# Performance work log

Hardware: AMD Instinct MI355X
Metric: run time of the kernel (lower is better)

Reference implementation:

```python
import jax, jax.numpy as jnp
import numpy as np
from jax import lax

D_MODEL = 768
D_STATE = 64
D_CONV = 4
EXPAND = 2
HEADDIM = 64
D_INNER = EXPAND * D_MODEL          # 1536
NHEADS = D_INNER // HEADDIM          # 24
NGROUPS = 1
CONV_DIM = D_INNER + 2 * NGROUPS * D_STATE      # 1664
D_IN_PROJ = 2 * D_INNER + 2 * NGROUPS * D_STATE + NHEADS  # 3224
EPS = 1e-5


def setup_inputs() -> dict:
    key = jax.random.key(0)
    ks = jax.random.split(key, 8)
    B, L = 2, 4096
    x = jax.random.normal(ks[0], (B, L, D_MODEL), jnp.float32)
    W_in = jax.random.normal(ks[1], (D_MODEL, D_IN_PROJ), jnp.float32) * (D_MODEL ** -0.5)
    conv_w = jax.random.normal(ks[2], (CONV_DIM, D_CONV), jnp.float32) * 0.2
    conv_b = jnp.zeros((CONV_DIM,), jnp.float32)
    # dt_bias so that softplus(dt_bias) ~ [1e-3, 1e-1], like mamba init
    dt = jax.random.uniform(ks[3], (NHEADS,), jnp.float32, 1e-3, 1e-1)
    dt_bias = dt + jnp.log(-jnp.expm1(-dt))
    A_log = jnp.log(jax.random.uniform(ks[4], (NHEADS,), jnp.float32, 1.0, 16.0))
    D = jnp.ones((NHEADS,), jnp.float32)
    norm_w = jnp.ones((D_INNER,), jnp.float32)
    W_out = jax.random.normal(ks[5], (D_INNER, D_MODEL), jnp.float32) * (D_INNER ** -0.5)
    return {"x": x, "W_in": W_in, "conv_w": conv_w, "conv_b": conv_b,
            "dt_bias": dt_bias, "A_log": A_log, "D": D,
            "norm_w": norm_w, "W_out": W_out}


def _mamba2(x, W_in, conv_w, conv_b, dt_bias, A_log, D, norm_w, W_out):
    B, L, _ = x.shape
    zxbcdt = x @ W_in                                  # (B,L,3224)
    z = zxbcdt[..., :D_INNER]                          # gate
    xBC = zxbcdt[..., D_INNER:D_INNER + CONV_DIM]
    dt = zxbcdt[..., D_INNER + CONV_DIM:]              # (B,L,H)
    dt = jax.nn.softplus(dt + dt_bias)

    # causal depthwise conv1d, kernel D_CONV, then SiLU
    xp = jnp.pad(xBC, ((0, 0), (D_CONV - 1, 0), (0, 0)))
    conv = sum(xp[:, k:k + L, :] * conv_w[:, k] for k in range(D_CONV))
    xBC = jax.nn.silu(conv + conv_b)

    xs = xBC[..., :D_INNER].reshape(B, L, NHEADS, HEADDIM)
    Bm = xBC[..., D_INNER:D_INNER + D_STATE]           # (B,L,N)
    Cm = xBC[..., D_INNER + D_STATE:]                  # (B,L,N)

    A = -jnp.exp(A_log)                                # (H,)
    dA = jnp.exp(dt * A)                               # (B,L,H)

    def step(h, inp):
        dA_t, dt_t, x_t, B_t, C_t = inp
        # h: (B,H,P,N)
        h = h * dA_t[:, :, None, None] \
            + (dt_t[:, :, None] * x_t)[..., None] * B_t[:, None, None, :]
        y = jnp.einsum('bhpn,bn->bhp', h, C_t)
        return h, y

    inps = (jnp.moveaxis(dA, 1, 0), jnp.moveaxis(dt, 1, 0),
            jnp.moveaxis(xs, 1, 0), jnp.moveaxis(Bm, 1, 0),
            jnp.moveaxis(Cm, 1, 0))
    h0 = jnp.zeros((B, NHEADS, HEADDIM, D_STATE), x.dtype)
    _, ys = lax.scan(step, h0, inps)                   # (L,B,H,P)
    y = jnp.moveaxis(ys, 0, 1) + D[None, None, :, None] * xs
    y = y.reshape(B, L, D_INNER)

    # gated RMSNorm: norm(y * silu(z)) * norm_w
    y = y * jax.nn.silu(z)
    y = y * lax.rsqrt(jnp.mean(y * y, axis=-1, keepdims=True) + EPS) * norm_w
    return y @ W_out


def reference(x, W_in, conv_w, conv_b, dt_bias, A_log, D, norm_w, W_out):
    return _mamba2(x, W_in, conv_w, conv_b, dt_bias, A_log, D, norm_w, W_out)
```

## Files before the change

kernel.cpp:

```cpp
#include <hip/hip_runtime.h>

#define B_   2
#define L_   4096
#define DM   768
#define DI   1536
#define DS   64
#define H_   24
#define P_   64
#define CD   1664
#define NPJ  3224
#define N1   3200
#define Q_   64
#define NC   64
#define SP   76
#define HS   72
#define WDS  772
#define CROWS 16

typedef short          bf16x8 __attribute__((ext_vector_type(8)));
typedef _Float16       f16x8  __attribute__((ext_vector_type(8)));
typedef _Float16       f16x4  __attribute__((ext_vector_type(4)));
typedef unsigned short us8    __attribute__((ext_vector_type(8)));
typedef unsigned short us4    __attribute__((ext_vector_type(4)));
typedef float          f32x4  __attribute__((ext_vector_type(4)));

__device__ __forceinline__ unsigned short f2bf(float f) {
  unsigned u = __float_as_uint(f);
  u += 0x7fffu + ((u >> 16) & 1u);
  return (unsigned short)(u >> 16);
}
__device__ __forceinline__ float bf2f(unsigned short u) {
  return __uint_as_float(((unsigned)u) << 16);
}
__device__ __forceinline__ float siluf(float x) { return x / (1.f + expf(-x)); }
__device__ __forceinline__ float softplusf(float x) { return (x > 20.f) ? x : log1pf(expf(x)); }

__device__ __forceinline__ void gload16(const unsigned short* g, unsigned short* l) {
  __builtin_amdgcn_global_load_lds(
      (const __attribute__((address_space(1))) void*)g,
      (__attribute__((address_space(3))) void*)l, 16, 0, 0);
}

__global__ __launch_bounds__(256)
void k_transpose_cast(const float* __restrict__ src, unsigned short* __restrict__ dst,
                      int R, int C)
{
  __shared__ float tile[32][33];
  const int tx = threadIdx.x & 31, ty = threadIdx.x >> 5;
  const int r0 = blockIdx.x * 32, c0 = blockIdx.y * 32;
#pragma unroll
  for (int r = 0; r < 4; ++r) {
    int rr = r0 + ty + r * 8, cc = c0 + tx;
    if (rr < R && cc < C) tile[ty + r * 8][tx] = src[(size_t)rr * C + cc];
  }
  __syncthreads();
#pragma unroll
  for (int r = 0; r < 4; ++r) {
    int orow = c0 + ty + r * 8, ocol = r0 + tx;
    if (orow < C && ocol < R) dst[(size_t)orow * R + ocol] = f2bf(tile[tx][ty + r * 8]);
  }
}

__global__ void k_wdtT(const float* __restrict__ W_in, float* __restrict__ WdtT)
{
  const int idx = blockIdx.x * 256 + threadIdx.x;
  if (idx >= H_ * DM) return;
  const int k = idx / H_, h = idx % H_;
  WdtT[(size_t)h * DM + k] = W_in[(size_t)k * NPJ + N1 + h];
}

template<int BM, int BN, int WM, int WN, bool OUT_BF16>
__global__ __launch_bounds__((BM / WM) * (BN / WN) * 64)
void k_gemm_t(const unsigned short* __restrict__ A, const unsigned short* __restrict__ Bt,
              void* __restrict__ C0v, int ld0, int ncol0,
              void* __restrict__ C1v, int ld1, int K)
{
  constexpr int MI = WM / 16, NI = WN / 16;
  constexpr int WAVES_N = BN / WN;
  constexpr int T  = (BM / WM) * (BN / WN) * 64;
  constexpr int RG = T / 8;
  constexpr int RA = BM / RG, RB = BN / RG;
  const int m0 = blockIdx.x * BM, n0 = blockIdx.y * BN;
  __shared__ unsigned short As[BM][64];
  __shared__ unsigned short Bs[BN][64];
  const int tid  = threadIdx.x;
  const int wave = tid >> 6, lane = tid & 63;
  const int quad = lane >> 4, r16 = lane & 15;
  const int wm = (wave / WAVES_N) * WM, wn = (wave % WAVES_N) * WN;

  const int lr8 = lane >> 3;
  const int csw = ((lane & 7) ^ lr8) * 8;
  const unsigned short* gA = A  + (size_t)(m0 + wave * 8 + lr8) * K + csw;
  const unsigned short* gB = Bt + (size_t)(n0 + wave * 8 + lr8) * K + csw;
  unsigned short* lA = &As[wave * 8][0] + (size_t)lane * 8;
  unsigned short* lB = &Bs[wave * 8][0] + (size_t)lane * 8;

  f32x4 acc[MI][NI];
#pragma unroll
  for (int mi = 0; mi < MI; ++mi)
#pragma unroll
    for (int ni = 0; ni < NI; ++ni) acc[mi][ni] = (f32x4){0.f, 0.f, 0.f, 0.f};

  for (int k0 = 0; k0 < K; k0 += 64) {
#pragma unroll
    for (int r = 0; r < RA; ++r)
      gload16(gA + (size_t)(r * RG) * K + k0, lA + (size_t)r * RG * 64);
#pragma unroll
    for (int r = 0; r < RB; ++r)
      gload16(gB + (size_t)(r * RG) * K + k0, lB + (size_t)r * RG * 64);
    __syncthreads();
    bf16x8 af[MI][2], bfr[NI][2];
#pragma unroll
    for (int mi = 0; mi < MI; ++mi)
#pragma unroll
      for (int ks = 0; ks < 2; ++ks)
        af[mi][ks] = *(const bf16x8*)&As[wm + mi * 16 + r16][((quad + ks * 4) ^ (r16 & 7)) * 8];
#pragma unroll
    for (int ni = 0; ni < NI; ++ni)
#pragma unroll
      for (int ks = 0; ks < 2; ++ks)
        bfr[ni][ks] = *(const bf16x8*)&Bs[wn + ni * 16 + r16][((quad + ks * 4) ^ (r16 & 7)) * 8];
#pragma unroll
    for (int mi = 0; mi < MI; ++mi)
#pragma unroll
      for (int ni = 0; ni < NI; ++ni)
#pragma unroll
        for (int ks = 0; ks < 2; ++ks)
          acc[mi][ni] = __builtin_amdgcn_mfma_f32_16x16x32_bf16(
              af[mi][ks], bfr[ni][ks], acc[mi][ni], 0, 0, 0);
    __syncthreads();
  }
#pragma unroll
  for (int mi = 0; mi < MI; ++mi)
#pragma unroll
    for (int ni = 0; ni < NI; ++ni) {
      int col = n0 + wn + ni * 16 + r16;
      void* dst; int ld, c;
      if (col < ncol0) { dst = C0v; ld = ld0; c = col; }
      else             { dst = C1v; ld = ld1; c = col - ncol0; }
#pragma unroll
      for (int r = 0; r < 4; ++r) {
        int row = m0 + wm + mi * 16 + quad * 4 + r;
        if (OUT_BF16) ((unsigned short*)dst)[(size_t)row * ld + c] = f2bf(acc[mi][ni][r]);
        else          ((float*)dst)[(size_t)row * ld + c] = acc[mi][ni][r];
      }
    }
}

__global__ __launch_bounds__(256)
void k_conv2(const unsigned short* __restrict__ xbc, const float* __restrict__ cw,
             const float* __restrict__ cb, _Float16* __restrict__ xs,
             float* __restrict__ Bm, float* __restrict__ Cm)
{
  const int ch = blockIdx.x * 256 + threadIdx.x;
  if (ch >= CD) return;
  const int r0 = blockIdx.y * CROWS;
  const float w0 = cw[ch * 4], w1 = cw[ch * 4 + 1], w2 = cw[ch * 4 + 2], w3 = cw[ch * 4 + 3];
  const float bias = cb[ch];
  float a, b, c;
  if ((r0 & (L_ - 1)) == 0) {
    a = 0.f; b = 0.f; c = 0.f;
  } else {
    a = bf2f(xbc[(size_t)(r0 - 3) * CD + ch]);
    b = bf2f(xbc[(size_t)(r0 - 2) * CD + ch]);
    c = bf2f(xbc[(size_t)(r0 - 1) * CD + ch]);
  }
#pragma unroll
  for (int i = 0; i < CROWS; ++i) {
    const int lr = r0 + i;
    float d = bf2f(xbc[(size_t)lr * CD + ch]);
    float v = siluf(bias + a * w0 + b * w1 + c * w2 + d * w3);
    a = b; b = c; c = d;
    if (ch < DI)           xs[(size_t)lr * DI + ch] = (_Float16)v;
    else if (ch < DI + DS) Bm[(size_t)lr * DS + (ch - DI)] = v;
    else                   Cm[(size_t)lr * DS + (ch - DI - DS)] = v;
  }
}

__global__ __launch_bounds__(384)
void k_dt2(const float* __restrict__ x, const float* __restrict__ WdtT,
           const float* __restrict__ dt_bias, float* __restrict__ dtv,
           unsigned short* __restrict__ xb)
{
  __shared__ float sW[H_][WDS];
  for (int i = threadIdx.x; i < H_ * DM; i += 384)
    sW[i / DM][i % DM] = WdtT[i];
  const int h = threadIdx.x % H_, rloc = threadIdx.x / H_;
  const int lrow = blockIdx.x * 16 + rloc;
  const float* xr = x + (size_t)lrow * DM;
  __syncthreads();
  float acc = 0.f;
#pragma unroll 8
  for (int k = 0; k < DM; k += 4) {
    f32x4 xv = *(const f32x4*)(xr + k);
    f32x4 wv = *(const f32x4*)&sW[h][k];
    acc += xv[0] * wv[0] + xv[1] * wv[1] + xv[2] * wv[2] + xv[3] * wv[3];
  }
  dtv[(size_t)lrow * H_ + h] = softplusf(acc + dt_bias[h]);
  const float* xi = xr + h * 32;
  unsigned short* xo = xb + (size_t)lrow * DM + h * 32;
#pragma unroll
  for (int j = 0; j < 32; j += 8) {
    f32x4 a = *(const f32x4*)(xi + j);
    f32x4 b = *(const f32x4*)(xi + j + 4);
    us8 o;
#pragma unroll
    for (int e = 0; e < 4; ++e) { o[e] = f2bf(a[e]); o[e + 4] = f2bf(b[e]); }
    *(us8*)(xo + j) = o;
  }
}

__global__ __launch_bounds__(256)
void k_intra(const _Float16* __restrict__ xs, const float* __restrict__ Bm,
             const float* __restrict__ Cm, const float* __restrict__ dtv,
             const float* __restrict__ A_log, const float* __restrict__ Dp,
             float* __restrict__ cumA, _Float16* __restrict__ ytot,
             _Float16* __restrict__ Sbuf)
{
  const int c = blockIdx.x, h = blockIdx.y, bz = blockIdx.z;
  const int gidx = (bz * H_ + h) * NC + c;
  __shared__ _Float16 sCW[Q_][HS];
  __shared__ _Float16 sB [Q_][HS];
  __shared__ _Float16 sBT[Q_][HS];
  __shared__ _Float16 sXT[Q_][HS];
  __shared__ float scum[Q_], sdt[Q_];
  const int tid = threadIdx.x;
  const int rowbase = bz * L_ + c * Q_;

  {
    const int j = tid >> 2, s16 = (tid & 3) * 16;
    if (tid < Q_) {
      const float dtval = dtv[(size_t)(rowbase + tid) * H_ + h];
      sdt[tid] = dtval;
      const float A = -expf(A_log[h]);
      float v = dtval;
#pragma unroll
      for (int off = 1; off < 64; off <<= 1) {
        float o = __shfl_up(v, off, 64);
        if (tid >= off) v += o;
      }
      v *= A;
      scum[tid] = v;
      cumA[(size_t)gidx * Q_ + tid] = v;
    }
    const _Float16* xsrc = xs + (size_t)(rowbase + j) * DI + h * P_ + s16;
    f16x8 xv0 = *(const f16x8*)xsrc;
    f16x8 xv1 = *(const f16x8*)(xsrc + 8);
    f32x4 bv[4], cv[4];
    const float* bsrc = Bm + (size_t)(rowbase + j) * DS + s16;
    const float* csrc = Cm + (size_t)(rowbase + j) * DS + s16;
#pragma unroll
    for (int q = 0; q < 4; ++q) {
      bv[q] = *(const f32x4*)(bsrc + q * 4);
      cv[q] = *(const f32x4*)(csrc + q * 4);
    }
    __syncthreads();
    const float coef = expf(scum[Q_ - 1] - scum[j]) * sdt[j];
    union { f16x8 v; _Float16 e[8]; } pc[2], pb[2];
#pragma unroll
    for (int q = 0; q < 4; ++q)
#pragma unroll
      for (int e = 0; e < 4; ++e) {
        int o = q * 4 + e;
        pc[o >> 3].e[o & 7] = (_Float16)cv[q][e];
        pb[o >> 3].e[o & 7] = (_Float16)bv[q][e];
        sBT[s16 + o][j] = (_Float16)(bv[q][e] * coef);
        sXT[s16 + o][j] = (o < 8) ? xv0[o] : xv1[o - 8];
      }
    *(f16x8*)&sCW[j][s16]     = pc[0].v;
    *(f16x8*)&sCW[j][s16 + 8] = pc[1].v;
    *(f16x8*)&sB [j][s16]     = pb[0].v;
    *(f16x8*)&sB [j][s16 + 8] = pb[1].v;
  }
  __syncthreads();

  const int wave = tid >> 6, lane = tid & 63;
  const int quad = lane >> 4, r16 = lane & 15;
  const int i0 = wave * 16;
  const int irow = i0 + quad * 4;

  f32x4 g[4];
#pragma unroll
  for (int q = 0; q < 4; ++q) g[q] = (f32x4){0.f, 0.f, 0.f, 0.f};
#pragma unroll
  for (int ni = 0; ni < 4; ++ni) {
    if (ni <= wave) {
#pragma unroll
      for (int ks = 0; ks < 2; ++ks)
        g[ni] = __builtin_amdgcn_mfma_f32_16x16x32_f16(
            *(const f16x8*)&sCW[i0 + r16][ks * 32 + quad * 8],
            *(const f16x8*)&sB [ni * 16 + r16][ks * 32 + quad * 8], g[ni], 0, 0, 0);
    }
  }
  float wv[4][4];
#pragma unroll
  for (int ni = 0; ni < 4; ++ni)
#pragma unroll
    for (int r = 0; r < 4; ++r) {
      int i = irow + r, jcol = ni * 16 + r16;
      float v = 0.f;
      if (ni <= wave && jcol <= i)
        v = g[ni][r] * expf(scum[i] - scum[jcol]) * sdt[jcol];
      wv[ni][r] = v;
    }
  __syncthreads();
#pragma unroll
  for (int ni = 0; ni < 4; ++ni)
#pragma unroll
    for (int r = 0; r < 4; ++r)
      sCW[irow + r][ni * 16 + r16] = (_Float16)wv[ni][r];
  __syncthreads();

  const float Dh = Dp[h];
  f32x4 y[4];
#pragma unroll
  for (int q = 0; q < 4; ++q) y[q] = (f32x4){0.f, 0.f, 0.f, 0.f};
#pragma unroll
  for (int ni = 0; ni < 4; ++ni)
#pragma unroll
    for (int ks = 0; ks < 2; ++ks) {
      if (ks == 0 || wave >= 2)
        y[ni] = __builtin_amdgcn_mfma_f32_16x16x32_f16(
            *(const f16x8*)&sCW[i0 + r16][ks * 32 + quad * 8],
            *(const f16x8*)&sXT[ni * 16 + r16][ks * 32 + quad * 8], y[ni], 0, 0, 0);
    }
#pragma unroll
  for (int ni = 0; ni < 4; ++ni)
#pragma unroll
    for (int r = 0; r < 4; ++r) {
      const float xval = (float)sXT[ni * 16 + r16][irow + r];
      ytot[(size_t)(rowbase + irow + r) * DI + h * P_ + ni * 16 + r16] =
          (_Float16)(y[ni][r] + Dh * xval);
    }

  f32x4 t4[4];
#pragma unroll
  for (int q = 0; q < 4; ++q) t4[q] = (f32x4){0.f, 0.f, 0.f, 0.f};
#pragma unroll
  for (int ni = 0; ni < 4; ++ni)
#pragma unroll
    for (int ks = 0; ks < 2; ++ks)
      t4[ni] = __builtin_amdgcn_mfma_f32_16x16x32_f16(
          *(const f16x8*)&sBT[i0 + r16][ks * 32 + quad * 8],
          *(const f16x8*)&sXT[ni * 16 + r16][ks * 32 + quad * 8], t4[ni], 0, 0, 0);
  _Float16* sp = Sbuf + (size_t)gidx * (DS * P_);
#pragma unroll
  for (int ni = 0; ni < 4; ++ni)
#pragma unroll
    for (int r = 0; r < 4; ++r)
      sp[(irow + r) * P_ + ni * 16 + r16] = (_Float16)t4[ni][r];
}

__global__ __launch_bounds__(64)
void k_chunkscan(_Float16* __restrict__ Sbuf, const float* __restrict__ cumA)
{
  const int seg = blockIdx.x, h = blockIdx.y, bz = blockIdx.z;
  const int bh = bz * H_ + h;
  __shared__ float dec[NC];
  const int tid = threadIdx.x;
  dec[tid] = expf(cumA[((size_t)(bh * NC + tid)) * Q_ + (Q_ - 1)]);
  __syncthreads();
  _Float16* base = Sbuf + (size_t)bh * NC * (DS * P_) + (size_t)seg * 256 + (size_t)tid * 4;
  float s[4] = {0.f, 0.f, 0.f, 0.f};
  f16x4 bA[8], bB[8];
#pragma unroll
  for (int j = 0; j < 8; ++j) bA[j] = *(const f16x4*)(base + (size_t)j * (DS * P_));
#pragma unroll
  for (int g = 0; g < 8; ++g) {
    if (g + 1 < 8) {
#pragma unroll
      for (int j = 0; j < 8; ++j) {
        f16x4 v = *(const f16x4*)(base + (size_t)((g + 1) * 8 + j) * (DS * P_));
        if (g & 1) bA[j] = v; else bB[j] = v;
      }
    }
#pragma unroll
    for (int j = 0; j < 8; ++j) {
      const int c = g * 8 + j;
      f16x4 cur = (g & 1) ? bB[j] : bA[j];
      f16x4 sto;
#pragma unroll
      for (int e = 0; e < 4; ++e) sto[e] = (_Float16)s[e];
      *(f16x4*)(base + (size_t)c * (DS * P_)) = sto;
      const float d = dec[c];
#pragma unroll
      for (int e = 0; e < 4; ++e) s[e] = s[e] * d + (float)cur[e];
    }
  }
}

__global__ __launch_bounds__(256)
void k_inter(const float* __restrict__ Cm, const float* __restrict__ cumA,
             const _Float16* __restrict__ Sbuf, _Float16* __restrict__ ytot)
{
  const int c = blockIdx.x, h = blockIdx.y, bz = blockIdx.z;
  const int gidx = (bz * H_ + h) * NC + c;
  __shared__ float sS[DS][SP];
  __shared__ float sC[Q_][SP];
  __shared__ float scum[Q_];
  const int tid = threadIdx.x;
  const int jr = tid >> 2, blk = (tid & 3) * 16;
  const int rowbase = bz * L_ + c * Q_;
  {
    const _Float16* ssrc = Sbuf + (size_t)gidx * (DS * P_) + jr * P_ + blk;
    f16x8 sv0 = *(const f16x8*)ssrc;
    f16x8 sv1 = *(const f16x8*)(ssrc + 8);
    const float* csrc = Cm + (size_t)(rowbase + jr) * DS + blk;
#pragma unroll
    for (int o = 0; o < 8; ++o) {
      sS[jr][blk + o]     = (float)sv0[o];
      sS[jr][blk + 8 + o] = (float)sv1[o];
    }
#pragma unroll
    for (int q = 0; q < 4; ++q)
      *(f32x4*)&sC[jr][blk + q * 4] = *(const f32x4*)(csrc + q * 4);
    if (tid < Q_) scum[tid] = cumA[(size_t)gidx * Q_ + tid];
  }
  __syncthreads();
  const int i = jr;
  f32x4 acc[4];
#pragma unroll
  for (int q = 0; q < 4; ++q) acc[q] = (f32x4){0.f, 0.f, 0.f, 0.f};
  for (int n = 0; n < DS; ++n) {
    float cv = sC[i][n];
#pragma unroll
    for (int q = 0; q < 4; ++q) acc[q] += cv * *(const f32x4*)&sS[n][blk + q * 4];
  }
  const float e = expf(scum[i]);
  _Float16* yt = ytot + (size_t)(rowbase + i) * DI + h * P_ + blk;
  f16x8 y0 = *(const f16x8*)yt;
  f16x8 y1 = *(const f16x8*)(yt + 8);
#pragma unroll
  for (int o = 0; o < 16; ++o) {
    float cur = (float)((o < 8) ? y0[o] : y1[o - 8]);
    cur += e * acc[o >> 2][o & 3];
    if (o < 8) y0[o] = (_Float16)cur; else y1[o - 8] = (_Float16)cur;
  }
  *(f16x8*)yt = y0;
  *(f16x8*)(yt + 8) = y1;
}

__global__ __launch_bounds__(192)
void k_rms(const unsigned short* __restrict__ z, const _Float16* __restrict__ ytot,
           const float* __restrict__ norm_w, unsigned short* __restrict__ ynorm)
{
  const int row = blockIdx.x, tid = threadIdx.x;
  const int e0 = tid * 8;
  us8 zv = *(const us8*)(z + (size_t)row * DI + e0);
  f16x8 yv = *(const f16x8*)(ytot + (size_t)row * DI + e0);
  float g[8];
  float ss = 0.f;
#pragma unroll
  for (int q = 0; q < 8; ++q) {
    g[q] = (float)yv[q] * siluf(bf2f(zv[q]));
    ss += g[q] * g[q];
  }
#pragma unroll
  for (int off = 32; off > 0; off >>= 1) ss += __shfl_down(ss, off);
  __shared__ float wsum[3];
  __shared__ float sscale;
  if ((tid & 63) == 0) wsum[tid >> 6] = ss;
  __syncthreads();
  if (tid == 0) sscale = rsqrtf((wsum[0] + wsum[1] + wsum[2]) * (1.f / DI) + 1e-5f);
  __syncthreads();
  const float sc = sscale;
  us8 o;
#pragma unroll
  for (int q = 0; q < 8; ++q) o[q] = f2bf(g[q] * sc * norm_w[e0 + q]);
  *(us8*)(ynorm + (size_t)row * DI + e0) = o;
}

extern "C" void kernel_launch(void* const* d_in, const int* in_sizes, int n_in,
                              void* d_out, int out_size, void* d_ws, size_t ws_size,
                              hipStream_t stream)
{
  (void)in_sizes; (void)n_in; (void)out_size;
  const float* x       = (const float*)d_in[0];
  const float* W_in    = (const float*)d_in[1];
  const float* conv_w  = (const float*)d_in[2];
  const float* conv_b  = (const float*)d_in[3];
  const float* dt_bias = (const float*)d_in[4];
  const float* A_log   = (const float*)d_in[5];
  const float* Dp      = (const float*)d_in[6];
  const float* norm_w  = (const float*)d_in[7];
  const float* W_out   = (const float*)d_in[8];
  float* out = (float*)d_out;

  const int nb = ((size_t)2 * L_ * 16320 + 7385088 <= ws_size) ? 2 : 1;
  const int rows = nb * L_;

  char* ws = (char*)d_ws;
  unsigned short* zseg = (unsigned short*)ws;  ws += (size_t)rows * DI * 2;
  unsigned short* xbc  = (unsigned short*)ws;  ws += (size_t)rows * CD * 2;
  _Float16* xs   = (_Float16*)ws;  ws += (size_t)rows * DI * 2;
  _Float16* ytot = (_Float16*)ws;  ws += (size_t)rows * DI * 2;
  float* Bm   = (float*)ws;  ws += (size_t)rows * DS * 4;
  float* Cm   = (float*)ws;  ws += (size_t)rows * DS * 4;
  float* dtv  = (float*)ws;  ws += (size_t)rows * H_ * 4;
  float* cumA = (float*)ws;  ws += (size_t)rows * H_ * 4;
  _Float16* Sbuf = (_Float16*)ws;  ws += (size_t)rows * 3072;
  unsigned short* WinT  = (unsigned short*)ws; ws += (size_t)NPJ * DM * 2;
  unsigned short* WoutT = (unsigned short*)ws; ws += (size_t)DM * DI * 2;
  float* WdtT   = (float*)ws;  ws += (size_t)H_ * DM * 4;
  unsigned short* xb    = (unsigned short*)Sbuf;
  unsigned short* ynorm = (unsigned short*)xs;

  k_transpose_cast<<<dim3(24, (NPJ + 31) / 32), 256, 0, stream>>>(W_in, WinT, DM, NPJ);
  k_transpose_cast<<<dim3(48, 24), 256, 0, stream>>>(W_out, WoutT, DI, DM);
  k_wdtT<<<(H_ * DM + 255) / 256, 256, 0, stream>>>(W_in, WdtT);

  for (int b0 = 0; b0 < B_; b0 += nb) {
    const float* xp = x + (size_t)b0 * L_ * DM;

    k_dt2<<<rows / 16, 384, 0, stream>>>(xp, WdtT, dt_bias, dtv, xb);
    k_gemm_t<256, 128, 64, 64, true><<<dim3(rows / 256, N1 / 128), 512, 0, stream>>>(
        xb, WinT, zseg, DI, DI, xbc, CD, DM);
    k_conv2<<<dim3(7, rows / CROWS), 256, 0, stream>>>(xbc, conv_w, conv_b, xs, Bm, Cm);
    k_intra<<<dim3(NC, H_, nb), 256, 0, stream>>>(xs, Bm, Cm, dtv, A_log, Dp, cumA, ytot, Sbuf);
    k_chunkscan<<<dim3(16, H_, nb), 64, 0, stream>>>(Sbuf, cumA);
    k_inter<<<dim3(NC, H_, nb), 256, 0, stream>>>(Cm, cumA, Sbuf, ytot);
    k_rms<<<rows, 192, 0, stream>>>(zseg, ytot, norm_w, ynorm);
    k_gemm_t<128, 64, 64, 32, false><<<dim3(rows / 128, DM / 64), 256, 0, stream>>>(
        ynorm, WoutT, out + (size_t)b0 * L_ * DM, DM, DM, out + (size_t)b0 * L_ * DM, DM, DI);
  }
}
```

Baseline: 310.0 us.

## Fuse x-channel causal conv and SiLU into the intra-chunk kernel

The depthwise conv plus SiLU for the 1536 x channels moves out of k_conv2 and into k_intra. k_intra now loads four bf16 rows of xbc per position and computes the conv in registers before writing sXT. k_conv2 now only handles the 128 B/C channels. This removes the write and re-read of the intermediate fp16 xs buffer. In exchange, k_intra reads overlapping halo rows and spends more ALU time in its load phase.

Result: no change. 311.3 us (+0.4%).

```diff
diff --git a/kernel.cpp b/kernel.cpp
--- a/kernel.cpp
+++ b/kernel.cpp
@@ -147,14 +147,12 @@
     }
 }
 
-__global__ __launch_bounds__(256)
+__global__ __launch_bounds__(128)
 void k_conv2(const unsigned short* __restrict__ xbc, const float* __restrict__ cw,
-             const float* __restrict__ cb, _Float16* __restrict__ xs,
-             float* __restrict__ Bm, float* __restrict__ Cm)
-{
-  const int ch = blockIdx.x * 256 + threadIdx.x;
-  if (ch >= CD) return;
-  const int r0 = blockIdx.y * CROWS;
+             const float* __restrict__ cb, float* __restrict__ Bm, float* __restrict__ Cm)
+{
+  const int ch = DI + threadIdx.x;
+  const int r0 = blockIdx.x * CROWS;
   const float w0 = cw[ch * 4], w1 = cw[ch * 4 + 1], w2 = cw[ch * 4 + 2], w3 = cw[ch * 4 + 3];
   const float bias = cb[ch];
   float a, b, c;
@@ -171,9 +169,8 @@
     float d = bf2f(xbc[(size_t)lr * CD + ch]);
     float v = siluf(bias + a * w0 + b * w1 + c * w2 + d * w3);
     a = b; b = c; c = d;
-    if (ch < DI)           xs[(size_t)lr * DI + ch] = (_Float16)v;
-    else if (ch < DI + DS) Bm[(size_t)lr * DS + (ch - DI)] = v;
-    else                   Cm[(size_t)lr * DS + (ch - DI - DS)] = v;
+    if (threadIdx.x < DS) Bm[(size_t)lr * DS + threadIdx.x] = v;
+    else                  Cm[(size_t)lr * DS + (threadIdx.x - DS)] = v;
   }
 }
 
@@ -211,7 +208,8 @@
 }
 
 __global__ __launch_bounds__(256)
-void k_intra(const _Float16* __restrict__ xs, const float* __restrict__ Bm,
+void k_intra(const unsigned short* __restrict__ xbc, const float* __restrict__ cw,
+             const float* __restrict__ cb, const float* __restrict__ Bm,
              const float* __restrict__ Cm, const float* __restrict__ dtv,
              const float* __restrict__ A_log, const float* __restrict__ Dp,
              float* __restrict__ cumA, _Float16* __restrict__ ytot,
@@ -224,8 +222,11 @@
   __shared__ _Float16 sBT[Q_][HS];
   __shared__ _Float16 sXT[Q_][HS];
   __shared__ float scum[Q_], sdt[Q_];
+  __shared__ float scw[4][Q_];
+  __shared__ float scb[Q_];
   const int tid = threadIdx.x;
   const int rowbase = bz * L_ + c * Q_;
+  const int ch0 = h * P_;
 
   {
     const int j = tid >> 2, s16 = (tid & 3) * 16;
@@ -243,9 +244,22 @@
       scum[tid] = v;
       cumA[(size_t)gidx * Q_ + tid] = v;
     }
-    const _Float16* xsrc = xs + (size_t)(rowbase + j) * DI + h * P_ + s16;
-    f16x8 xv0 = *(const f16x8*)xsrc;
-    f16x8 xv1 = *(const f16x8*)(xsrc + 8);
+    scw[tid & 3][tid >> 2] = cw[(size_t)ch0 * 4 + tid];
+    if (tid < Q_) scb[tid] = cb[ch0 + tid];
+    us8 xr[4][2];
+    const int rbz = bz * L_;
+#pragma unroll
+    for (int d = 0; d < 4; ++d) {
+      const int rr = rowbase + j - 3 + d;
+      const int rc = (rr < rbz) ? rbz : rr;
+      const unsigned short* src = xbc + (size_t)rc * CD + ch0 + s16;
+      xr[d][0] = *(const us8*)src;
+      xr[d][1] = *(const us8*)(src + 8);
+      if (rr < rbz) {
+        us8 z8 = {0, 0, 0, 0, 0, 0, 0, 0};
+        xr[d][0] = z8; xr[d][1] = z8;
+      }
+    }
     f32x4 bv[4], cv[4];
     const float* bsrc = Bm + (size_t)(rowbase + j) * DS + s16;
     const float* csrc = Cm + (size_t)(rowbase + j) * DS + s16;
@@ -262,10 +276,17 @@
 #pragma unroll
       for (int e = 0; e < 4; ++e) {
         int o = q * 4 + e;
+        const int cc = s16 + o;
         pc[o >> 3].e[o & 7] = (_Float16)cv[q][e];
         pb[o >> 3].e[o & 7] = (_Float16)bv[q][e];
-        sBT[s16 + o][j] = (_Float16)(bv[q][e] * coef);
-        sXT[s16 + o][j] = (o < 8) ? xv0[o] : xv1[o - 8];
+        sBT[cc][j] = (_Float16)(bv[q][e] * coef);
+        float a0 = bf2f(xr[0][o >> 3][o & 7]);
+        float a1 = bf2f(xr[1][o >> 3][o & 7]);
+        float a2 = bf2f(xr[2][o >> 3][o & 7]);
+        float a3 = bf2f(xr[3][o >> 3][o & 7]);
+        float v = scb[cc] + a0 * scw[0][cc] + a1 * scw[1][cc]
+                          + a2 * scw[2][cc] + a3 * scw[3][cc];
+        sXT[cc][j] = (_Float16)siluf(v);
       }
     *(f16x8*)&sCW[j][s16]     = pc[0].v;
     *(f16x8*)&sCW[j][s16 + 8] = pc[1].v;
@@ -515,8 +536,9 @@
     k_dt2<<<rows / 16, 384, 0, stream>>>(xp, WdtT, dt_bias, dtv, xb);
     k_gemm_t<256, 128, 64, 64, true><<<dim3(rows / 256, N1 / 128), 512, 0, stream>>>(
         xb, WinT, zseg, DI, DI, xbc, CD, DM);
-    k_conv2<<<dim3(7, rows / CROWS), 256, 0, stream>>>(xbc, conv_w, conv_b, xs, Bm, Cm);
-    k_intra<<<dim3(NC, H_, nb), 256, 0, stream>>>(xs, Bm, Cm, dtv, A_log, Dp, cumA, ytot, Sbuf);
+    k_conv2<<<rows / CROWS, 128, 0, stream>>>(xbc, conv_w, conv_b, Bm, Cm);
+    k_intra<<<dim3(NC, H_, nb), 256, 0, stream>>>(xbc, conv_w, conv_b, Bm, Cm, dtv,
+                                                  A_log, Dp, cumA, ytot, Sbuf);
     k_chunkscan<<<dim3(16, H_, nb), 64, 0, stream>>>(Sbuf, cumA);
     k_inter<<<dim3(NC, H_, nb), 256, 0, stream>>>(Cm, cumA, Sbuf, ytot);
     k_rms<<<rows, 192, 0, stream>>>(zseg, ytot, norm_w, ynorm);
```
